# Optimization experiments

Hardware: AMD Instinct MI355X
Metric: run time of the kernel (lower is better)

## Reference

```python
import jax, jax.numpy as jnp
import numpy as np

N = 50000
IN_CH = 128
HID = 64
HEADS = 4
OUT_CH = 2
E = 800000
NEG_SLOPE = 0.2


def setup_inputs() -> dict:
    key = jax.random.key(0)
    ks = jax.random.split(key, 10)
    x = jax.random.normal(ks[0], (N, IN_CH), dtype=jnp.float32)
    edge_index = jax.random.randint(ks[1], (2, E), 0, N, dtype=jnp.int64)
    # layer 1: GATConv(IN_CH -> HID, heads=HEADS, concat=True)
    s1 = 1.0 / np.sqrt(IN_CH)
    W1 = jax.random.normal(ks[2], (IN_CH, HEADS * HID), dtype=jnp.float32) * s1
    a_src1 = jax.random.normal(ks[3], (HEADS, HID), dtype=jnp.float32) * (1.0 / np.sqrt(HID))
    a_dst1 = jax.random.normal(ks[4], (HEADS, HID), dtype=jnp.float32) * (1.0 / np.sqrt(HID))
    b1 = jnp.zeros((HEADS * HID,), dtype=jnp.float32)
    # layer 2: GATConv(HEADS*HID -> OUT_CH, heads=1, concat=False)
    s2 = 1.0 / np.sqrt(HEADS * HID)
    W2 = jax.random.normal(ks[5], (HEADS * HID, OUT_CH), dtype=jnp.float32) * s2
    a_src2 = jax.random.normal(ks[6], (1, OUT_CH), dtype=jnp.float32) * (1.0 / np.sqrt(OUT_CH))
    a_dst2 = jax.random.normal(ks[7], (1, OUT_CH), dtype=jnp.float32) * (1.0 / np.sqrt(OUT_CH))
    b2 = jnp.zeros((OUT_CH,), dtype=jnp.float32)
    return {"x": x, "edge_index": edge_index, "W1": W1, "a_src1": a_src1,
            "a_dst1": a_dst1, "b1": b1, "W2": W2, "a_src2": a_src2,
            "a_dst2": a_dst2, "b2": b2}


def gat_conv(x, W, a_src, a_dst, bias, src, dst, heads, ch, concat):
    n = x.shape[0]
    h = (x @ W).reshape(n, heads, ch)                       # [N,H,C]
    al_s = jnp.sum(h * a_src[None], axis=-1)                # [N,H]
    al_d = jnp.sum(h * a_dst[None], axis=-1)                # [N,H]
    e = al_s[src] + al_d[dst]                               # [E,H]
    e = jnp.where(e > 0, e, NEG_SLOPE * e)                  # leaky_relu
    # segment softmax over edges grouped by destination node
    m = jax.ops.segment_max(e, dst, num_segments=n)         # [N,H]
    m = jnp.where(jnp.isfinite(m), m, 0.0)
    p = jnp.exp(e - m[dst])                                 # [E,H]
    denom = jax.ops.segment_sum(p, dst, num_segments=n)     # [N,H]
    alpha = p / (denom[dst] + 1e-16)                        # [E,H]
    msg = h[src] * alpha[:, :, None]                        # [E,H,C]
    out = jax.ops.segment_sum(msg, dst, num_segments=n)     # [N,H,C]
    if concat:
        out = out.reshape(n, heads * ch) + bias
    else:
        out = out.mean(axis=1) + bias
    return out


def reference(x, edge_index, W1, a_src1, a_dst1, b1, W2, a_src2, a_dst2, b2):
    n = x.shape[0]
    # PyG GATConv default: add self-loops
    loops = jnp.arange(n, dtype=edge_index.dtype)
    src = jnp.concatenate([edge_index[0], loops])
    dst = jnp.concatenate([edge_index[1], loops])
    h = gat_conv(x, W1, a_src1, a_dst1, b1, src, dst, HEADS, HID, True)
    h = jax.nn.relu(h)
    out = gat_conv(h, W2, a_src2, a_dst2, b2, src, dst, 1, OUT_CH, False)
    return out
```

## Files before the change

kernel.cpp:

```cpp
#include <hip/hip_runtime.h>

#define NNODE 50000
#define NEDGE 800000
#define NTOT  (NEDGE + NNODE)
#define NB_SCAN 49
#define NGEMM 1564

typedef __attribute__((ext_vector_type(8))) short bf16x8;
typedef __attribute__((ext_vector_type(4))) float f32x4;
union U4B8 { uint4 u; bf16x8 b; };

__device__ __forceinline__ unsigned short f2bf(float f) {
  union { float f; unsigned u; } v; v.f = f;
  unsigned r = v.u + 0x7FFFu + ((v.u >> 16) & 1u);
  return (unsigned short)(r >> 16);
}
__device__ __forceinline__ float bflo(unsigned u) {
  union { unsigned u; float f; } v; v.u = u << 16; return v.f;
}
__device__ __forceinline__ float bfhi(unsigned u) {
  union { unsigned u; float f; } v; v.u = u & 0xFFFF0000u; return v.f;
}
__device__ __forceinline__ unsigned packbf(float a, float b) {
  return (unsigned)f2bf(a) | ((unsigned)f2bf(b) << 16);
}

__global__ __launch_bounds__(256) void k_prep(const float* __restrict__ W1,
                                              unsigned short* __restrict__ W1bT,
                                              int* __restrict__ deg) {
  const int b = (int)blockIdx.x;
  if (b < 32) {
    int flat = b * 256 + threadIdx.x;
    int k = flat >> 6, c4 = (flat & 63) << 2;
    float4 v = *(const float4*)(W1 + k * 256 + c4);
    W1bT[(c4 + 0) * 128 + k] = f2bf(v.x);
    W1bT[(c4 + 1) * 128 + k] = f2bf(v.y);
    W1bT[(c4 + 2) * 128 + k] = f2bf(v.z);
    W1bT[(c4 + 3) * 128 + k] = f2bf(v.w);
  } else {
    int i = (b - 32) * 256 + threadIdx.x;
    if (i < NNODE) deg[i] = 0;
  }
}

__global__ __launch_bounds__(256) void k_gemm_deg(
    const float* __restrict__ x, const unsigned short* __restrict__ W1bT,
    const float* __restrict__ a_s1, const float* __restrict__ a_d1,
    unsigned short* __restrict__ h1b, float* __restrict__ als1,
    float* __restrict__ ald1, const int* __restrict__ ei,
    int* __restrict__ deg, int* __restrict__ rank) {
  __shared__ unsigned short xs[64 * 136];
  if ((int)blockIdx.x >= NGEMM) {
    int i = ((int)blockIdx.x - NGEMM) * 256 + threadIdx.x;
    if (i < NTOT) {
      int d = (i < NEDGE) ? ei[NEDGE + i] : (i - NEDGE);
      rank[i] = atomicAdd(deg + d, 1);
    }
    return;
  }
  const int t = threadIdx.x;
  const int rb = (int)blockIdx.x >> 1, nhalf = (int)blockIdx.x & 1;
  const int grow0 = rb * 64;
#pragma unroll
  for (int i = 0; i < 8; ++i) {
    int f = t + i * 256;
    int row = f >> 5, c4 = (f & 31) << 2;
    int gr = grow0 + row;
    float4 v = make_float4(0.f, 0.f, 0.f, 0.f);
    if (gr < NNODE) v = *(const float4*)(x + gr * 128 + c4);
    *(uint2*)(xs + row * 136 + c4) = make_uint2(packbf(v.x, v.y), packbf(v.z, v.w));
  }
  const int wid = t >> 6, lane = t & 63;
  const int wrow = (wid >> 1) * 32;
  const int head = nhalf * 2 + (wid & 1);
  const int c_lo = lane & 15, g = lane >> 4;
  U4B8 bfr[4][4];
#pragma unroll
  for (int nr = 0; nr < 4; ++nr) {
    int c = head * 64 + nr * 16 + c_lo;
#pragma unroll
    for (int ks = 0; ks < 4; ++ks)
      bfr[nr][ks].u = *(const uint4*)(W1bT + c * 128 + ks * 32 + g * 8);
  }
  __syncthreads();
  U4B8 afr[2][4];
#pragma unroll
  for (int mr = 0; mr < 2; ++mr)
#pragma unroll
    for (int ks = 0; ks < 4; ++ks)
      afr[mr][ks].u = *(const uint4*)(xs + (wrow + mr * 16 + c_lo) * 136 + ks * 32 + g * 8);
  f32x4 acc[2][4];
#pragma unroll
  for (int mr = 0; mr < 2; ++mr)
#pragma unroll
    for (int nr = 0; nr < 4; ++nr) acc[mr][nr] = (f32x4){0.f, 0.f, 0.f, 0.f};
#pragma unroll
  for (int ks = 0; ks < 4; ++ks)
#pragma unroll
    for (int mr = 0; mr < 2; ++mr)
#pragma unroll
      for (int nr = 0; nr < 4; ++nr)
        acc[mr][nr] = __builtin_amdgcn_mfma_f32_16x16x32_bf16(
            afr[mr][ks].b, bfr[nr][ks].b, acc[mr][nr], 0, 0, 0);
  float as_v[4], ad_v[4];
#pragma unroll
  for (int nr = 0; nr < 4; ++nr) {
    as_v[nr] = a_s1[head * 64 + nr * 16 + c_lo];
    ad_v[nr] = a_d1[head * 64 + nr * 16 + c_lo];
  }
  float ps[2][4], pd[2][4];
#pragma unroll
  for (int mr = 0; mr < 2; ++mr)
#pragma unroll
    for (int r = 0; r < 4; ++r) {
      float s = 0.f, dsum = 0.f;
#pragma unroll
      for (int nr = 0; nr < 4; ++nr) {
        s += acc[mr][nr][r] * as_v[nr];
        dsum += acc[mr][nr][r] * ad_v[nr];
      }
      ps[mr][r] = s; pd[mr][r] = dsum;
    }
#pragma unroll
  for (int m = 1; m < 16; m <<= 1)
#pragma unroll
    for (int mr = 0; mr < 2; ++mr)
#pragma unroll
      for (int r = 0; r < 4; ++r) {
        ps[mr][r] += __shfl_xor(ps[mr][r], m, 64);
        pd[mr][r] += __shfl_xor(pd[mr][r], m, 64);
      }
  if (c_lo == 0) {
#pragma unroll
    for (int mr = 0; mr < 2; ++mr)
#pragma unroll
      for (int r = 0; r < 4; ++r) {
        int node = grow0 + wrow + mr * 16 + g * 4 + r;
        if (node < NNODE) {
          als1[node * 4 + head] = ps[mr][r];
          ald1[node * 4 + head] = pd[mr][r];
        }
      }
  }
  __syncthreads();
  unsigned short* tb = xs + wid * 2048;
#pragma unroll
  for (int mr = 0; mr < 2; ++mr)
#pragma unroll
    for (int nr = 0; nr < 4; ++nr)
#pragma unroll
      for (int r = 0; r < 4; ++r)
        tb[(mr * 16 + g * 4 + r) * 64 + nr * 16 + c_lo] = f2bf(acc[mr][nr][r]);
#pragma unroll
  for (int i = 0; i < 4; ++i) {
    int unit = i * 64 + lane;
    int row = unit >> 3, cS = (unit & 7) * 8;
    int node = grow0 + wrow + row;
    if (node < NNODE) {
      uint4 v = *(const uint4*)(tb + unit * 8);
      *(uint4*)(h1b + (size_t)node * 256 + nhalf * 128 + (wid & 1) * 64 + cS) = v;
    }
  }
}

__global__ __launch_bounds__(1024) void k_scan1(const int* __restrict__ deg,
                                                int* __restrict__ rowp,
                                                int* __restrict__ bsum) {
  __shared__ int sh[1024];
  const int t = threadIdx.x;
  const int idx = (int)blockIdx.x * 1024 + t;
  int v = (idx < NNODE) ? deg[idx] : 0;
  sh[t] = v;
  __syncthreads();
#pragma unroll
  for (int off = 1; off < 1024; off <<= 1) {
    int add = (t >= off) ? sh[t - off] : 0;
    __syncthreads();
    sh[t] += add;
    __syncthreads();
  }
  if (idx < NNODE) rowp[idx + 1] = sh[t];
  if (t == 1023) bsum[blockIdx.x] = sh[1023];
}

__global__ __launch_bounds__(256) void k_scanscatter(
    const int* __restrict__ ei, const int* __restrict__ rowp,
    const int* __restrict__ bsum, const int* __restrict__ rank,
    int* __restrict__ rowf, int* __restrict__ esrc) {
  __shared__ int boff[64];
  const int t = threadIdx.x;
  if (t < 64) {
    int v = (t < NB_SCAN) ? bsum[t] : 0;
    int orig = v;
#pragma unroll
    for (int off = 1; off < 64; off <<= 1) {
      int n = __shfl_up(v, off, 64);
      if (t >= off) v += n;
    }
    boff[t] = v - orig;
  }
  __syncthreads();
  const int i = (int)blockIdx.x * 256 + t;
  if (i < NNODE) {
    rowf[i + 1] = rowp[i + 1] + boff[i >> 10];
    if (i == 0) rowf[0] = 0;
  }
  if (i < NTOT) {
    int s, d;
    if (i < NEDGE) { s = ei[i]; d = ei[NEDGE + i]; }
    else           { s = i - NEDGE; d = s; }
    int base = (d == 0) ? 0 : rowp[d] + boff[(d - 1) >> 10];
    esrc[base + rank[i]] = s;
  }
}

__global__ __launch_bounds__(256) void k_agg1(
    const unsigned short* __restrict__ h1b, const float* __restrict__ als1,
    const float* __restrict__ ald1, const int* __restrict__ rowptr,
    const int* __restrict__ esrc, const float* __restrict__ b1,
    const float* __restrict__ W2, const float* __restrict__ a_s2,
    const float* __restrict__ a_d2, float4* __restrict__ h2c) {
  const int w = threadIdx.x >> 6, lane = threadIdx.x & 63;
  const int d = (int)blockIdx.x * 4 + w;
  const int half = lane >> 5, cl = lane & 31;
  const int head = cl >> 3;
  const float ald = ald1[d * 4 + head];
  const int begin = rowptr[d], end = rowptr[d + 1];
  float acc[8];
#pragma unroll
  for (int i = 0; i < 8; ++i) acc[i] = 0.f;
  float S = 0.f;

  int j = begin + half;
  int s = (j < end) ? esrc[j] : -1;
  while (s >= 0) {
    const uint4 hv = *(const uint4*)(h1b + (size_t)s * 256 + cl * 8);
    float e = als1[s * 4 + head] + ald;
    int jn = j + 2;
    int sn = (jn < end) ? esrc[jn] : -1;
    e = fmaxf(e, 0.2f * e);
    float wgt = __expf(e);
    S += wgt;
    acc[0] += wgt * bflo(hv.x); acc[1] += wgt * bfhi(hv.x);
    acc[2] += wgt * bflo(hv.y); acc[3] += wgt * bfhi(hv.y);
    acc[4] += wgt * bflo(hv.z); acc[5] += wgt * bfhi(hv.z);
    acc[6] += wgt * bflo(hv.w); acc[7] += wgt * bfhi(hv.w);
    j = jn; s = sn;
  }
  S += __shfl_xor(S, 32, 64);
#pragma unroll
  for (int i = 0; i < 8; ++i) acc[i] += __shfl_xor(acc[i], 32, 64);

  const float inv = 1.f / S;
  const int c0 = cl * 8;
  float4 ba = *(const float4*)(b1 + c0);
  float4 bb = *(const float4*)(b1 + c0 + 4);
  float bias[8] = {ba.x, ba.y, ba.z, ba.w, bb.x, bb.y, bb.z, bb.w};
  float4 w0 = *(const float4*)(W2 + c0 * 2);
  float4 w1 = *(const float4*)(W2 + c0 * 2 + 4);
  float4 w2 = *(const float4*)(W2 + c0 * 2 + 8);
  float4 w3 = *(const float4*)(W2 + c0 * 2 + 12);
  float wa[16] = {w0.x, w0.y, w0.z, w0.w, w1.x, w1.y, w1.z, w1.w,
                  w2.x, w2.y, w2.z, w2.w, w3.x, w3.y, w3.z, w3.w};
  float p0 = 0.f, p1 = 0.f;
#pragma unroll
  for (int i = 0; i < 8; ++i) {
    float v = acc[i] * inv + bias[i];
    v = v > 0.f ? v : 0.f;
    p0 += v * wa[2 * i];
    p1 += v * wa[2 * i + 1];
  }
#pragma unroll
  for (int m = 1; m < 32; m <<= 1) {
    p0 += __shfl_xor(p0, m, 64);
    p1 += __shfl_xor(p1, m, 64);
  }
  if (lane == 0) {
    h2c[d] = make_float4(p0, p1,
                         p0 * a_s2[0] + p1 * a_s2[1],
                         p0 * a_d2[0] + p1 * a_d2[1]);
  }
}

__global__ __launch_bounds__(256) void k_agg2(
    const float4* __restrict__ h2c, const int* __restrict__ rowptr,
    const int* __restrict__ esrc, const float* __restrict__ b2,
    float* __restrict__ out) {
  int d = (int)blockIdx.x * 256 + threadIdx.x;
  if (d >= NNODE) return;
  const float ald = h2c[d].w;
  const int begin = rowptr[d], end = rowptr[d + 1];
  float S = 0.f, a0 = 0.f, a1 = 0.f;
  for (int j = begin; j < end; ++j) {
    int s = esrc[j];
    float4 v = h2c[s];
    float e = v.z + ald;
    e = fmaxf(e, 0.2f * e);
    float wgt = __expf(e);
    S += wgt;
    a0 += wgt * v.x;
    a1 += wgt * v.y;
  }
  float inv = 1.f / S;
  out[d * 2 + 0] = a0 * inv + b2[0];
  out[d * 2 + 1] = a1 * inv + b2[1];
}

static inline size_t algn(size_t x) { return (x + 255) & ~(size_t)255; }

extern "C" void kernel_launch(void* const* d_in, const int* in_sizes, int n_in,
                              void* d_out, int out_size, void* d_ws, size_t ws_size,
                              hipStream_t stream) {
  const float* x    = (const float*)d_in[0];
  const int*   ei   = (const int*)d_in[1];
  const float* W1   = (const float*)d_in[2];
  const float* a_s1 = (const float*)d_in[3];
  const float* a_d1 = (const float*)d_in[4];
  const float* b1   = (const float*)d_in[5];
  const float* W2   = (const float*)d_in[6];
  const float* a_s2 = (const float*)d_in[7];
  const float* a_d2 = (const float*)d_in[8];
  const float* b2   = (const float*)d_in[9];
  float* out = (float*)d_out;

  char* w = (char*)d_ws;
  size_t o = 0;
  unsigned short* h1b = (unsigned short*)(w + o); o += algn((size_t)NNODE * 256 * 2);
  unsigned short* W1bT = (unsigned short*)(w + o); o += algn((size_t)256 * 128 * 2);
  float* als1 = (float*)(w + o); o += algn((size_t)NNODE * 4 * 4);
  float* ald1 = (float*)(w + o); o += algn((size_t)NNODE * 4 * 4);
  int*   deg  = (int*)(w + o);   o += algn((size_t)NNODE * 4);
  int*   rowp = (int*)(w + o);   o += algn((size_t)(NNODE + 1) * 4);
  int*   rowf = (int*)(w + o);   o += algn((size_t)(NNODE + 1) * 4);
  int*   rank = (int*)(w + o);   o += algn((size_t)NTOT * 4);
  int*   esrc = (int*)(w + o);   o += algn((size_t)NTOT * 4);
  int*   bsum = (int*)(w + o);   o += 256;
  float4* h2c = (float4*)(w + o); o += algn((size_t)NNODE * 16);
  (void)ws_size; (void)n_in; (void)in_sizes; (void)out_size;

  k_prep<<<dim3(32 + 196), dim3(256), 0, stream>>>(W1, W1bT, deg);
  k_gemm_deg<<<dim3(NGEMM + (NTOT + 255) / 256), dim3(256), 0, stream>>>(
      x, W1bT, a_s1, a_d1, h1b, als1, ald1, ei, deg, rank);
  k_scan1<<<dim3(NB_SCAN), dim3(1024), 0, stream>>>(deg, rowp, bsum);
  k_scanscatter<<<dim3((NTOT + 255) / 256), dim3(256), 0, stream>>>(
      ei, rowp, bsum, rank, rowf, esrc);
  k_agg1<<<dim3(12500), dim3(256), 0, stream>>>(h1b, als1, ald1, rowf, esrc, b1,
                                                W2, a_s2, a_d2, h2c);
  k_agg2<<<dim3((NNODE + 255) / 256), dim3(256), 0, stream>>>(h2c, rowf, esrc, b2, out);
}
```

Measured before the change: 227.9 us.

## Widen GEMM blocks, use wave-shuffle scan, and split agg2 edges across lanes

The GEMM kernel now uses 512-thread blocks that cover all four heads for 64 rows, so each block loads the x tile once instead of twice. The degree scan switches from a 1024-thread shared-memory Hillis-Steele scan to 256-element chunks built with wave shuffles, and the block-offset prefix now handles 196 chunks. The second-layer aggregation assigns four lanes per destination node and combines them with shuffle reductions, which cuts serial per-thread edge loops. The trade-offs are higher register and LDS pressure per GEMM block and more threads in agg2.

```diff
diff --git a/kernel.cpp b/kernel.cpp
--- a/kernel.cpp
+++ b/kernel.cpp
@@ -3,8 +3,9 @@
 #define NNODE 50000
 #define NEDGE 800000
 #define NTOT  (NEDGE + NNODE)
-#define NB_SCAN 49
-#define NGEMM 1564
+#define NCHUNK 196
+#define NGEMM 782
+#define NDEG 1661
 
 typedef __attribute__((ext_vector_type(8))) short bf16x8;
 typedef __attribute__((ext_vector_type(4))) float f32x4;
@@ -43,27 +44,26 @@
   }
 }
 
-__global__ __launch_bounds__(256) void k_gemm_deg(
+__global__ __launch_bounds__(512) void k_gemm_deg(
     const float* __restrict__ x, const unsigned short* __restrict__ W1bT,
     const float* __restrict__ a_s1, const float* __restrict__ a_d1,
     unsigned short* __restrict__ h1b, float* __restrict__ als1,
     float* __restrict__ ald1, const int* __restrict__ ei,
     int* __restrict__ deg, int* __restrict__ rank) {
-  __shared__ unsigned short xs[64 * 136];
+  __shared__ unsigned short xs[16384];
+  const int t = threadIdx.x;
   if ((int)blockIdx.x >= NGEMM) {
-    int i = ((int)blockIdx.x - NGEMM) * 256 + threadIdx.x;
+    int i = ((int)blockIdx.x - NGEMM) * 512 + t;
     if (i < NTOT) {
       int d = (i < NEDGE) ? ei[NEDGE + i] : (i - NEDGE);
       rank[i] = atomicAdd(deg + d, 1);
     }
     return;
   }
-  const int t = threadIdx.x;
-  const int rb = (int)blockIdx.x >> 1, nhalf = (int)blockIdx.x & 1;
-  const int grow0 = rb * 64;
-#pragma unroll
-  for (int i = 0; i < 8; ++i) {
-    int f = t + i * 256;
+  const int grow0 = (int)blockIdx.x * 64;
+#pragma unroll
+  for (int i = 0; i < 4; ++i) {
+    int f = t + i * 512;
     int row = f >> 5, c4 = (f & 31) << 2;
     int gr = grow0 + row;
     float4 v = make_float4(0.f, 0.f, 0.f, 0.f);
@@ -71,8 +71,8 @@
     *(uint2*)(xs + row * 136 + c4) = make_uint2(packbf(v.x, v.y), packbf(v.z, v.w));
   }
   const int wid = t >> 6, lane = t & 63;
-  const int wrow = (wid >> 1) * 32;
-  const int head = nhalf * 2 + (wid & 1);
+  const int wrow = (wid >> 2) * 32;
+  const int head = wid & 3;
   const int c_lo = lane & 15, g = lane >> 4;
   U4B8 bfr[4][4];
 #pragma unroll
@@ -158,58 +158,69 @@
     int node = grow0 + wrow + row;
     if (node < NNODE) {
       uint4 v = *(const uint4*)(tb + unit * 8);
-      *(uint4*)(h1b + (size_t)node * 256 + nhalf * 128 + (wid & 1) * 64 + cS) = v;
+      *(uint4*)(h1b + (size_t)node * 256 + head * 64 + cS) = v;
     }
   }
 }
 
-__global__ __launch_bounds__(1024) void k_scan1(const int* __restrict__ deg,
-                                                int* __restrict__ rowp,
-                                                int* __restrict__ bsum) {
-  __shared__ int sh[1024];
-  const int t = threadIdx.x;
-  const int idx = (int)blockIdx.x * 1024 + t;
-  int v = (idx < NNODE) ? deg[idx] : 0;
-  sh[t] = v;
+__global__ __launch_bounds__(256) void k_scan1(const int* __restrict__ deg,
+                                               int* __restrict__ rowp,
+                                               int* __restrict__ csum) {
+  __shared__ int ws[4];
+  const int t = threadIdx.x, lane = t & 63, wid = t >> 6;
+  const int idx = (int)blockIdx.x * 256 + t;
+  int sv = (idx < NNODE) ? deg[idx] : 0;
+#pragma unroll
+  for (int off = 1; off < 64; off <<= 1) {
+    int n = __shfl_up(sv, off, 64);
+    if (lane >= off) sv += n;
+  }
+  if (lane == 63) ws[wid] = sv;
   __syncthreads();
-#pragma unroll
-  for (int off = 1; off < 1024; off <<= 1) {
-    int add = (t >= off) ? sh[t - off] : 0;
-    __syncthreads();
-    sh[t] += add;
-    __syncthreads();
-  }
-  if (idx < NNODE) rowp[idx + 1] = sh[t];
-  if (t == 1023) bsum[blockIdx.x] = sh[1023];
+  int add = 0;
+#pragma unroll
+  for (int p = 0; p < 3; ++p) if (wid > p) add += ws[p];
+  sv += add;
+  if (idx < NNODE) rowp[idx + 1] = sv;
+  if (t == 255) csum[blockIdx.x] = sv;
 }
 
 __global__ __launch_bounds__(256) void k_scanscatter(
     const int* __restrict__ ei, const int* __restrict__ rowp,
-    const int* __restrict__ bsum, const int* __restrict__ rank,
+    const int* __restrict__ csum, const int* __restrict__ rank,
     int* __restrict__ rowf, int* __restrict__ esrc) {
-  __shared__ int boff[64];
+  __shared__ int boff[256];
   const int t = threadIdx.x;
   if (t < 64) {
-    int v = (t < NB_SCAN) ? bsum[t] : 0;
-    int orig = v;
+    const int c0 = t * 4;
+    int s0 = (c0 + 0 < NCHUNK) ? csum[c0 + 0] : 0;
+    int s1 = (c0 + 1 < NCHUNK) ? csum[c0 + 1] : 0;
+    int s2 = (c0 + 2 < NCHUNK) ? csum[c0 + 2] : 0;
+    int s3 = (c0 + 3 < NCHUNK) ? csum[c0 + 3] : 0;
+    int local = s0 + s1 + s2 + s3;
+    int sv = local;
 #pragma unroll
     for (int off = 1; off < 64; off <<= 1) {
-      int n = __shfl_up(v, off, 64);
-      if (t >= off) v += n;
+      int n = __shfl_up(sv, off, 64);
+      if (t >= off) sv += n;
     }
-    boff[t] = v - orig;
+    int excl = sv - local;
+    boff[c0 + 0] = excl;
+    boff[c0 + 1] = excl + s0;
+    boff[c0 + 2] = excl + s0 + s1;
+    boff[c0 + 3] = excl + s0 + s1 + s2;
   }
   __syncthreads();
   const int i = (int)blockIdx.x * 256 + t;
   if (i < NNODE) {
-    rowf[i + 1] = rowp[i + 1] + boff[i >> 10];
+    rowf[i + 1] = rowp[i + 1] + boff[i >> 8];
     if (i == 0) rowf[0] = 0;
   }
   if (i < NTOT) {
     int s, d;
     if (i < NEDGE) { s = ei[i]; d = ei[NEDGE + i]; }
     else           { s = i - NEDGE; d = s; }
-    int base = (d == 0) ? 0 : rowp[d] + boff[(d - 1) >> 10];
+    int base = (d == 0) ? 0 : rowp[d] + boff[(d - 1) >> 8];
     esrc[base + rank[i]] = s;
   }
 }
@@ -286,12 +297,14 @@
     const float4* __restrict__ h2c, const int* __restrict__ rowptr,
     const int* __restrict__ esrc, const float* __restrict__ b2,
     float* __restrict__ out) {
-  int d = (int)blockIdx.x * 256 + threadIdx.x;
+  const int t = threadIdx.x;
+  const int g = t & 3;
+  const int d = (int)blockIdx.x * 64 + (t >> 2);
   if (d >= NNODE) return;
   const float ald = h2c[d].w;
   const int begin = rowptr[d], end = rowptr[d + 1];
   float S = 0.f, a0 = 0.f, a1 = 0.f;
-  for (int j = begin; j < end; ++j) {
+  for (int j = begin + g; j < end; j += 4) {
     int s = esrc[j];
     float4 v = h2c[s];
     float e = v.z + ald;
@@ -301,9 +314,14 @@
     a0 += wgt * v.x;
     a1 += wgt * v.y;
   }
-  float inv = 1.f / S;
-  out[d * 2 + 0] = a0 * inv + b2[0];
-  out[d * 2 + 1] = a1 * inv + b2[1];
+  S  += __shfl_xor(S, 1, 64);  S  += __shfl_xor(S, 2, 64);
+  a0 += __shfl_xor(a0, 1, 64); a0 += __shfl_xor(a0, 2, 64);
+  a1 += __shfl_xor(a1, 1, 64); a1 += __shfl_xor(a1, 2, 64);
+  if (g == 0) {
+    float inv = 1.f / S;
+    out[d * 2 + 0] = a0 * inv + b2[0];
+    out[d * 2 + 1] = a1 * inv + b2[1];
+  }
 }
 
 static inline size_t algn(size_t x) { return (x + 255) & ~(size_t)255; }
@@ -334,17 +352,17 @@
   int*   rowf = (int*)(w + o);   o += algn((size_t)(NNODE + 1) * 4);
   int*   rank = (int*)(w + o);   o += algn((size_t)NTOT * 4);
   int*   esrc = (int*)(w + o);   o += algn((size_t)NTOT * 4);
-  int*   bsum = (int*)(w + o);   o += 256;
+  int*   csum = (int*)(w + o);   o += 1024;
   float4* h2c = (float4*)(w + o); o += algn((size_t)NNODE * 16);
   (void)ws_size; (void)n_in; (void)in_sizes; (void)out_size;
 
   k_prep<<<dim3(32 + 196), dim3(256), 0, stream>>>(W1, W1bT, deg);
-  k_gemm_deg<<<dim3(NGEMM + (NTOT + 255) / 256), dim3(256), 0, stream>>>(
+  k_gemm_deg<<<dim3(NGEMM + NDEG), dim3(512), 0, stream>>>(
       x, W1bT, a_s1, a_d1, h1b, als1, ald1, ei, deg, rank);
-  k_scan1<<<dim3(NB_SCAN), dim3(1024), 0, stream>>>(deg, rowp, bsum);
+  k_scan1<<<dim3(NCHUNK), dim3(256), 0, stream>>>(deg, rowp, csum);
   k_scanscatter<<<dim3((NTOT + 255) / 256), dim3(256), 0, stream>>>(
-      ei, rowp, bsum, rank, rowf, esrc);
+      ei, rowp, csum, rank, rowf, esrc);
   k_agg1<<<dim3(12500), dim3(256), 0, stream>>>(h1b, als1, ald1, rowf, esrc, b1,
                                                 W2, a_s2, a_d2, h2c);
-  k_agg2<<<dim3((NNODE + 255) / 256), dim3(256), 0, stream>>>(h2c, rowf, esrc, b2, out);
-}
+  k_agg2<<<dim3((NNODE + 63) / 64), dim3(256), 0, stream>>>(h2c, rowf, esrc, b2, out);
+}
```

New measurement: 227.1 us. No clear change (-0.3%).
